# Kernel tuning notes

Hardware: AMD Instinct MI355X
Metric: run time of the kernel (lower is better)

The kernel has to match this reference:

```python
import jax, jax.numpy as jnp
import numpy as np

DIM = 2048
N_HEADS = 32
N_KV_HEADS = 8
HEAD_DIM = DIM // N_HEADS  # 64
N_REP = N_HEADS // N_KV_HEADS  # 4
B, S = 2, 2048
MASK_VAL = -32768.0


def setup_inputs() -> dict:
    key = jax.random.key(0)
    ks = jax.random.split(key, 7)
    x = jax.random.normal(ks[0], (B, S, DIM), dtype=jnp.float32)
    freqs_cos = jax.random.uniform(ks[1], (S, HEAD_DIM // 2), dtype=jnp.float32)
    freqs_sin = jax.random.uniform(ks[2], (S, HEAD_DIM // 2), dtype=jnp.float32)
    sc = 1.0 / np.sqrt(DIM)
    wq = jax.random.normal(ks[3], (N_HEADS * HEAD_DIM, DIM), dtype=jnp.float32) * sc
    wk = jax.random.normal(ks[4], (N_KV_HEADS * HEAD_DIM, DIM), dtype=jnp.float32) * sc
    wv = jax.random.normal(ks[5], (N_KV_HEADS * HEAD_DIM, DIM), dtype=jnp.float32) * sc
    wo = jax.random.normal(ks[6], (DIM, N_HEADS * HEAD_DIM), dtype=jnp.float32) * sc
    return {"x": x, "freqs_cos": freqs_cos, "freqs_sin": freqs_sin,
            "wq": wq, "wk": wk, "wv": wv, "wo": wo}


def _apply_rope(q, k, cos, sin):
    # q: [B,S,H,D], k: [B,S,Hkv,D]; interleaved real/imag pairs in last dim
    def rot(t):
        tr = t.reshape(t.shape[:-1] + (-1, 2))  # [..., D/2, 2]
        t_r, t_i = tr[..., 0], tr[..., 1]
        c = cos[None, :, None, :]  # broadcast over batch and heads
        s = sin[None, :, None, :]
        o_r = t_r * c - t_i * s
        o_i = t_r * s + t_i * c
        return jnp.stack([o_r, o_i], axis=-1).reshape(t.shape)
    return rot(q), rot(k)


def reference(x, freqs_cos, freqs_sin, wq, wk, wv, wo):
    bsz, seqlen, _ = x.shape
    xq = (x @ wq.T).reshape(bsz, seqlen, N_HEADS, HEAD_DIM)
    xk = (x @ wk.T).reshape(bsz, seqlen, N_KV_HEADS, HEAD_DIM)
    xv = (x @ wv.T).reshape(bsz, seqlen, N_KV_HEADS, HEAD_DIM)
    xq, xk = _apply_rope(xq, xk, freqs_cos, freqs_sin)
    # GQA: repeat each kv head n_rep times contiguously (matches per-head cat loop)
    xk = jnp.repeat(xk, N_REP, axis=2)  # [B,S,H,D]
    xv = jnp.repeat(xv, N_REP, axis=2)
    # [B,H,S,D]
    q = xq.transpose(0, 2, 1, 3)
    k = xk.transpose(0, 2, 1, 3)
    v = xv.transpose(0, 2, 1, 3)
    scores = jnp.einsum('bhqd,bhkd->bhqk', q, k) / jnp.sqrt(jnp.float32(HEAD_DIM))
    causal = jnp.triu(jnp.full((seqlen, seqlen), MASK_VAL, dtype=scores.dtype), k=1)
    scores = scores + causal[None, None, :, :]
    probs = jax.nn.softmax(scores.astype(jnp.float32), axis=-1).astype(q.dtype)
    out = jnp.einsum('bhqk,bhkd->bhqd', probs, v)
    out = out.transpose(0, 2, 1, 3).reshape(bsz, seqlen, -1)
    return out @ wo.T
```

## Files before the change

kernel.cpp:

```cpp
#include <hip/hip_runtime.h>
#include <hip/hip_bf16.h>
#include <type_traits>

typedef __bf16 bf16;
typedef __bf16 bf16x2 __attribute__((ext_vector_type(2)));
typedef __bf16 bf16x4 __attribute__((ext_vector_type(4)));
typedef __bf16 bf16x8 __attribute__((ext_vector_type(8)));
typedef float f32x4 __attribute__((ext_vector_type(4)));

#define AS1 __attribute__((address_space(1)))
#define AS3 __attribute__((address_space(3)))

#define KAPPA 0.180336880111f

__device__ __forceinline__ void load_lds16(const void* g, void* l) {
  __builtin_amdgcn_global_load_lds((AS1 void*)g, (AS3 void*)l, 16, 0, 0);
}
__device__ __forceinline__ float exp2_fast(float x) {
  return __builtin_amdgcn_exp2f(x);
}

__global__ void f2b_all(const float* __restrict__ x, const float* __restrict__ wq,
                        const float* __restrict__ wk, const float* __restrict__ wv,
                        const float* __restrict__ wo, bf16* __restrict__ xb,
                        bf16* __restrict__ wqkv, bf16* __restrict__ wob) {
  int bid = blockIdx.x;
  const float* src;
  bf16* dst;
  int off;
  if (bid < 8192) { src = x; dst = xb; off = bid; }
  else if (bid < 12288) { src = wq; dst = wqkv; off = bid - 8192; }
  else if (bid < 13312) { src = wk; dst = wqkv + 4194304; off = bid - 12288; }
  else if (bid < 14336) { src = wv; dst = wqkv + 5242880; off = bid - 13312; }
  else { src = wo; dst = wob; off = bid - 14336; }
  int i = (off * 256 + threadIdx.x) * 4;
  float4 v = *(const float4*)(src + i);
  bf16x4 o = {(bf16)v.x, (bf16)v.y, (bf16)v.z, (bf16)v.w};
  *(bf16x4*)(dst + i) = o;
}

__global__ __launch_bounds__(512, 2) void gemm_qkv(const bf16* __restrict__ A,
                                                   const bf16* __restrict__ Bw,
                                                   const float* __restrict__ fc,
                                                   const float* __restrict__ fs,
                                                   bf16* __restrict__ Qro,
                                                   bf16* __restrict__ Kro,
                                                   bf16* __restrict__ Vt) {
  const int K = 2048;
  __shared__ bf16 As[4][256][32];
  __shared__ bf16 Bs[4][256][32];
  const int t = threadIdx.x;
  const int wave = t >> 6, lane = t & 63, qd = lane >> 4, ln = lane & 15;
  const int wm = (wave >> 2) * 128;
  const int wn = (wave & 3) * 64;
  const int bn = blockIdx.x;
  const int bmrow = blockIdx.y * 256;

  const bf16* Ab = A + (size_t)bmrow * K;
  const bf16* Bb = Bw + (size_t)bn * 256 * K;

  auto stage = [&](const bf16* gb, char* lb, int tk, int sub) {
    int e = sub * 512 + t;
    int ro = e >> 2, gs = (e & 3) ^ (ro & 3);
    load_lds16(gb + (size_t)ro * K + tk * 32 + gs * 8,
               lb + (tk & 3) * 16384 + sub * 8192 + wave * 1024);
  };

#pragma unroll
  for (int tt = 0; tt < 3; tt++) {
    stage(Ab, (char*)As, tt, 0);
    stage(Ab, (char*)As, tt, 1);
    stage(Bb, (char*)Bs, tt, 0);
    stage(Bb, (char*)Bs, tt, 1);
  }
  asm volatile("s_waitcnt vmcnt(8)" ::: "memory");
  __builtin_amdgcn_s_barrier();

  f32x4 acc[8][4] = {};
  bf16x8 bfr[4];
  const int segoff = (qd ^ (ln & 3)) << 4;

  for (int tk = 0; tk < 64; tk++) {
    const char* Asl = (const char*)As + (tk & 3) * 16384;
    const char* Bsl = (const char*)Bs + (tk & 3) * 16384;

    bf16x8 af[4];
#pragma unroll
    for (int i = 0; i < 4; i++)
      af[i] = *(const bf16x8*)(Asl + (wm + i * 16 + ln) * 64 + segoff);
#pragma unroll
    for (int j = 0; j < 4; j++)
      bfr[j] = *(const bf16x8*)(Bsl + (wn + j * 16 + ln) * 64 + segoff);
    if (tk + 3 < 64) {
      stage(Ab, (char*)As, tk + 3, 0);
      stage(Ab, (char*)As, tk + 3, 1);
    }
    __builtin_amdgcn_s_barrier();
    asm volatile("s_waitcnt lgkmcnt(0)" ::: "memory");
    __builtin_amdgcn_sched_barrier(0);
    __builtin_amdgcn_s_setprio(1);
#pragma unroll
    for (int i = 0; i < 4; i++)
#pragma unroll
      for (int j = 0; j < 4; j++)
        acc[i][j] = __builtin_amdgcn_mfma_f32_16x16x32_bf16(af[i], bfr[j],
                                                            acc[i][j], 0, 0, 0);
    __builtin_amdgcn_s_setprio(0);
    __builtin_amdgcn_s_barrier();

#pragma unroll
    for (int i = 0; i < 4; i++)
      af[i] = *(const bf16x8*)(Asl + (wm + 64 + i * 16 + ln) * 64 + segoff);
    if (tk + 3 < 64) {
      stage(Bb, (char*)Bs, tk + 3, 0);
      stage(Bb, (char*)Bs, tk + 3, 1);
    }
    if (tk < 61) asm volatile("s_waitcnt vmcnt(8)" ::: "memory");
    else if (tk == 61) asm volatile("s_waitcnt vmcnt(4)" ::: "memory");
    else asm volatile("s_waitcnt vmcnt(0)" ::: "memory");
    __builtin_amdgcn_s_barrier();
    asm volatile("s_waitcnt lgkmcnt(0)" ::: "memory");
    __builtin_amdgcn_sched_barrier(0);
    __builtin_amdgcn_s_setprio(1);
#pragma unroll
    for (int i = 0; i < 4; i++)
#pragma unroll
      for (int j = 0; j < 4; j++)
        acc[4 + i][j] = __builtin_amdgcn_mfma_f32_16x16x32_bf16(
            af[i], bfr[j], acc[4 + i][j], 0, 0, 0);
    __builtin_amdgcn_s_setprio(0);
    __builtin_amdgcn_s_barrier();
  }

  const int b = bmrow >> 11;
  const int sb = (bmrow & 2047) + wm;
  const bool odd = ln & 1;

  if (bn < 10) {
    const bool isQ = bn < 8;
    const float kap = isQ ? KAPPA : 1.0f;
    const int h = (isQ ? bn : bn - 8) * 4 + (wave & 3);
    bf16* dst = isQ ? (Qro + (size_t)(b * 32 + h) * 2048 * 64)
                    : (Kro + (size_t)(b * 8 + h) * 2048 * 64);
#pragma unroll
    for (int i = 0; i < 8; i++) {
#pragma unroll
      for (int j = 0; j < 4; j++) {
        const int d = j * 16 + ln;
        const int i_f = d >> 1;
#pragma unroll
        for (int r = 0; r < 4; r++) {
          int s = sb + i * 16 + qd * 4 + r;
          float v = acc[i][j][r];
          float p = __shfl_xor(v, 1);
          float cv = fc[s * 32 + i_f] * kap;
          float sv = fs[s * 32 + i_f] * kap;
          float o = odd ? (p * sv + v * cv) : (v * cv - p * sv);
          dst[(size_t)s * 64 + d] = (bf16)o;
        }
      }
    }
  } else {
    const int kh = (bn - 10) * 4 + (wave & 3);
#pragma unroll
    for (int i = 0; i < 8; i++)
#pragma unroll
      for (int j = 0; j < 4; j++) {
        const int d = j * 16 + ln;
        int s = sb + i * 16 + qd * 4;
        bf16x4 ov = {(bf16)acc[i][j][0], (bf16)acc[i][j][1],
                     (bf16)acc[i][j][2], (bf16)acc[i][j][3]};
        *(bf16x4*)&Vt[((size_t)(b * 8 + kh) * 64 + d) * 2048 + s] = ov;
      }
  }
}

template <typename OutT>
__global__ __launch_bounds__(256, 4) void gemm_bt64(const bf16* __restrict__ A,
                                                    const bf16* __restrict__ Bw,
                                                    OutT* __restrict__ C,
                                                    int M, int N, int K) {
  __shared__ bf16 As[64][64];
  __shared__ bf16 Bs[128][64];
  const int t = threadIdx.x;
  const int wave = t >> 6, lane = t & 63, qd = lane >> 4, ln = lane & 15;
  const int wm = (wave >> 1) * 32;
  const int wn = (wave & 1) * 64;
  const size_t bm = (size_t)blockIdx.y * 64;
  const size_t bn = (size_t)blockIdx.x * 128;

  const bf16* Ab = A + bm * (size_t)K;
  const bf16* Bb = Bw + bn * (size_t)K;

  f32x4 acc[2][4] = {};

  for (int k0 = 0; k0 < K; k0 += 64) {
#pragma unroll
    for (int i = 0; i < 2; i++) {
      int e = i * 256 + t;
      int ro = e >> 3, gs = (e & 7) ^ (ro & 7);
      load_lds16(Ab + (size_t)ro * K + k0 + gs * 8,
                 (char*)As + i * 4096 + wave * 1024);
    }
#pragma unroll
    for (int i = 0; i < 4; i++) {
      int e = i * 256 + t;
      int ro = e >> 3, gs = (e & 7) ^ (ro & 7);
      load_lds16(Bb + (size_t)ro * K + k0 + gs * 8,
                 (char*)Bs + i * 4096 + wave * 1024);
    }
    __syncthreads();

#pragma unroll
    for (int kk = 0; kk < 2; kk++) {
      bf16x8 af[2], bfr[4];
#pragma unroll
      for (int i = 0; i < 2; i++) {
        int row = wm + i * 16 + ln;
        int ps = (kk * 4 + qd) ^ (row & 7);
        af[i] = *(const bf16x8*)((const char*)As + row * 128 + ps * 16);
      }
#pragma unroll
      for (int j = 0; j < 4; j++) {
        int row = wn + j * 16 + ln;
        int ps = (kk * 4 + qd) ^ (row & 7);
        bfr[j] = *(const bf16x8*)((const char*)Bs + row * 128 + ps * 16);
      }
#pragma unroll
      for (int i = 0; i < 2; i++)
#pragma unroll
        for (int j = 0; j < 4; j++)
          acc[i][j] = __builtin_amdgcn_mfma_f32_16x16x32_bf16(af[i], bfr[j],
                                                              acc[i][j], 0, 0, 0);
    }
    __syncthreads();
  }

#pragma unroll
  for (int i = 0; i < 2; i++)
#pragma unroll
    for (int j = 0; j < 4; j++)
#pragma unroll
      for (int r = 0; r < 4; r++) {
        size_t row = bm + wm + i * 16 + qd * 4 + r;
        size_t col = bn + wn + j * 16 + ln;
        C[row * N + col] = (OutT)acc[i][j][r];
      }
}

__global__ __launch_bounds__(256, 3) void attn_fwd(const bf16* __restrict__ Q,
                                                   const bf16* __restrict__ Kg,
                                                   const bf16* __restrict__ Vg,
                                                   bf16* __restrict__ O) {
  __shared__ bf16 Qs[128][64];
  __shared__ bf16 Ks[64][64];
  __shared__ bf16 Vs[64][64];
  __shared__ bf16 Ps[128][64];
  const int t = threadIdx.x;
  const int wave = t >> 6, lane = t & 63, qd = lane >> 4, ln = lane & 15;
  const int bid = blockIdx.x;
  const int qt = 15 - (bid >> 6);
  const int bh = bid & 63;
  const int b = bh >> 5, h = bh & 31, kh = h >> 2;
  const bf16* Qb = Q + ((size_t)(b * 32 + h) * 2048 + qt * 128) * 64;
  const bf16* Kb = Kg + (size_t)(b * 8 + kh) * 2048 * 64;
  const bf16* Vb = Vg + (size_t)(b * 8 + kh) * 64 * 2048;
  char* PsB = (char*)Ps;

#pragma unroll
  for (int i = 0; i < 4; i++) {
    int e = i * 256 + t;
    int row = e >> 3, sg = (e & 7) ^ (row & 7);
    load_lds16(Qb + (size_t)row * 64 + sg * 8, (char*)Qs + i * 4096 + wave * 1024);
  }

  f32x4 o_acc[4][2] = {};
  float l_st[2] = {0.f, 0.f};
  const int q0 = qt * 128 + wave * 32;
  const int nkb = 2 * qt + 2;

  for (int kb = 0; kb < nkb; kb++) {
    __syncthreads();
#pragma unroll
    for (int i = 0; i < 2; i++) {
      int e = i * 256 + t;
      int row = e >> 3, sg = (e & 7) ^ (row & 7);
      load_lds16(Kb + (size_t)(kb * 64 + row) * 64 + sg * 8,
                 (char*)Ks + i * 4096 + wave * 1024);
      load_lds16(Vb + (size_t)row * 2048 + kb * 64 + sg * 8,
                 (char*)Vs + i * 4096 + wave * 1024);
    }
    __syncthreads();

    f32x4 s_acc[4][2] = {};
#pragma unroll
    for (int kk = 0; kk < 2; kk++) {
      bf16x8 ak[4], bq[2];
#pragma unroll
      for (int j = 0; j < 4; j++) {
        int row = j * 16 + ln;
        int ph = (kk * 4 + qd) ^ (ln & 7);
        ak[j] = *(const bf16x8*)((const char*)Ks + row * 128 + ph * 16);
      }
#pragma unroll
      for (int mi = 0; mi < 2; mi++) {
        int row = wave * 32 + mi * 16 + ln;
        int ph = (kk * 4 + qd) ^ (ln & 7);
        bq[mi] = *(const bf16x8*)((const char*)Qs + row * 128 + ph * 16);
      }
#pragma unroll
      for (int j = 0; j < 4; j++)
#pragma unroll
        for (int mi = 0; mi < 2; mi++)
          s_acc[j][mi] = __builtin_amdgcn_mfma_f32_16x16x32_bf16(
              ak[j], bq[mi], s_acc[j][mi], 0, 0, 0);
    }

    auto smax = [&](auto maskc) {
      constexpr bool MASK = decltype(maskc)::value;
#pragma unroll
      for (int mi = 0; mi < 2; mi++) {
        const int qv = q0 + mi * 16 + ln;
        const int prow = wave * 32 + mi * 16 + ln;
        float rs = 0.f;
#pragma unroll
        for (int j = 0; j < 4; j++) {
          bf16x4 pk;
#pragma unroll
          for (int r = 0; r < 4; r++) {
            float s = s_acc[j][mi][r];
            if (MASK) {
              int k_glob = kb * 64 + j * 16 + qd * 4 + r;
              if (k_glob > qv) s = -1e5f;
            }
            float pv = exp2_fast(s - 16.f);
            rs += pv;
            pk[r] = (bf16)pv;
          }
          int ps = (j * 2 + (qd >> 1)) ^ (ln & 7);
          *(bf16x4*)(PsB + prow * 128 + ps * 16 + (qd & 1) * 8) = pk;
        }
        l_st[mi] += rs;
      }
    };
    if (kb * 64 + 63 > q0) smax(std::true_type{});
    else smax(std::false_type{});

#pragma unroll
    for (int kk = 0; kk < 2; kk++) {
      bf16x8 av[4], bp[2];
#pragma unroll
      for (int dj = 0; dj < 4; dj++) {
        int row = dj * 16 + ln;
        int ph = (kk * 4 + qd) ^ (ln & 7);
        av[dj] = *(const bf16x8*)((const char*)Vs + row * 128 + ph * 16);
      }
#pragma unroll
      for (int mi = 0; mi < 2; mi++) {
        int prow = wave * 32 + mi * 16 + ln;
        int ph = (kk * 4 + qd) ^ (ln & 7);
        bp[mi] = *(const bf16x8*)(PsB + prow * 128 + ph * 16);
      }
#pragma unroll
      for (int dj = 0; dj < 4; dj++)
#pragma unroll
        for (int mi = 0; mi < 2; mi++)
          o_acc[dj][mi] = __builtin_amdgcn_mfma_f32_16x16x32_bf16(
              av[dj], bp[mi], o_acc[dj][mi], 0, 0, 0);
    }
  }

#pragma unroll
  for (int mi = 0; mi < 2; mi++) {
    float lt = l_st[mi];
    lt += __shfl_xor(lt, 16);
    lt += __shfl_xor(lt, 32);
    float inv = 1.f / lt;
    int q_idx = qt * 128 + wave * 32 + mi * 16 + ln;
#pragma unroll
    for (int dj = 0; dj < 4; dj++) {
      bf16x4 ov;
#pragma unroll
      for (int r = 0; r < 4; r++) ov[r] = (bf16)(o_acc[dj][mi][r] * inv);
      *(bf16x4*)&O[((size_t)(b * 2048 + q_idx) * 32 + h) * 64 + dj * 16 + qd * 4] = ov;
    }
  }
}

extern "C" void kernel_launch(void* const* d_in, const int* in_sizes, int n_in,
                              void* d_out, int out_size, void* d_ws,
                              size_t ws_size, hipStream_t stream) {
  const float* x = (const float*)d_in[0];
  const float* fc = (const float*)d_in[1];
  const float* fs = (const float*)d_in[2];
  const float* wq = (const float*)d_in[3];
  const float* wk = (const float*)d_in[4];
  const float* wv = (const float*)d_in[5];
  const float* wo = (const float*)d_in[6];
  float* out = (float*)d_out;

  char* ws = (char*)d_ws;
  const size_t MB = (size_t)1 << 20;
  bf16* xb   = (bf16*)(ws + 0 * MB);
  bf16* wqkv = (bf16*)(ws + 16 * MB);
  bf16* wob  = (bf16*)(ws + 28 * MB);
  bf16* Qro  = (bf16*)(ws + 36 * MB);
  bf16* Kro  = (bf16*)(ws + 52 * MB);
  bf16* Vt   = (bf16*)(ws + 56 * MB);
  bf16* Oa   = (bf16*)(ws + 60 * MB);

  dim3 blk(256);
  f2b_all<<<18432, blk, 0, stream>>>(x, wq, wk, wv, wo, xb, wqkv, wob);
  gemm_qkv<<<dim3(12, 16), dim3(512), 0, stream>>>(xb, wqkv, fc, fs, Qro, Kro, Vt);
  attn_fwd<<<1024, blk, 0, stream>>>(Qro, Kro, Vt, Oa);
  gemm_bt64<float><<<dim3(16, 64), blk, 0, stream>>>(Oa, wob, out, 4096, 2048, 2048);
}
```

Baseline: 293.3 us.

## Shrink QKV GEMM N-tile to 192 to fill more CUs and change LDS swizzle

Result: faster. 273.8 us (-6.7%).

```diff
diff --git a/kernel.cpp b/kernel.cpp
--- a/kernel.cpp
+++ b/kernel.cpp
@@ -48,52 +48,61 @@
                                                    bf16* __restrict__ Vt) {
   const int K = 2048;
   __shared__ bf16 As[4][256][32];
-  __shared__ bf16 Bs[4][256][32];
+  __shared__ bf16 Bs[4][192][32];
   const int t = threadIdx.x;
   const int wave = t >> 6, lane = t & 63, qd = lane >> 4, ln = lane & 15;
   const int wm = (wave >> 2) * 128;
-  const int wn = (wave & 3) * 64;
+  const int wn = (wave & 3) * 48;
   const int bn = blockIdx.x;
   const int bmrow = blockIdx.y * 256;
 
   const bf16* Ab = A + (size_t)bmrow * K;
-  const bf16* Bb = Bw + (size_t)bn * 256 * K;
-
-  auto stage = [&](const bf16* gb, char* lb, int tk, int sub) {
+  const bf16* Bb = Bw + (size_t)bn * 192 * K;
+
+  auto stageA = [&](int tk, int sub) {
     int e = sub * 512 + t;
-    int ro = e >> 2, gs = (e & 3) ^ (ro & 3);
-    load_lds16(gb + (size_t)ro * K + tk * 32 + gs * 8,
-               lb + (tk & 3) * 16384 + sub * 8192 + wave * 1024);
+    int ro = e >> 2, gs = (e & 3) ^ ((ro >> 1) & 3);
+    load_lds16(Ab + (size_t)ro * K + tk * 32 + gs * 8,
+               (char*)As + (tk & 3) * 16384 + sub * 8192 + wave * 1024);
   };
+  auto stageB = [&](int tk, int sub) {
+    if (sub == 0 || t < 256) {
+      int e = sub * 512 + t;
+      int ro = e >> 2, gs = (e & 3) ^ ((ro >> 1) & 3);
+      load_lds16(Bb + (size_t)ro * K + tk * 32 + gs * 8,
+                 (char*)Bs + (tk & 3) * 12288 + sub * 8192 + wave * 1024);
+    }
+  };
 
 #pragma unroll
   for (int tt = 0; tt < 3; tt++) {
-    stage(Ab, (char*)As, tt, 0);
-    stage(Ab, (char*)As, tt, 1);
-    stage(Bb, (char*)Bs, tt, 0);
-    stage(Bb, (char*)Bs, tt, 1);
-  }
-  asm volatile("s_waitcnt vmcnt(8)" ::: "memory");
+    stageA(tt, 0);
+    stageA(tt, 1);
+    stageB(tt, 0);
+    stageB(tt, 1);
+  }
+  if (wave < 4) asm volatile("s_waitcnt vmcnt(8)" ::: "memory");
+  else         asm volatile("s_waitcnt vmcnt(6)" ::: "memory");
   __builtin_amdgcn_s_barrier();
 
-  f32x4 acc[8][4] = {};
-  bf16x8 bfr[4];
-  const int segoff = (qd ^ (ln & 3)) << 4;
+  f32x4 acc[8][3] = {};
+  bf16x8 bfr[3];
+  const int segoff = (qd ^ ((ln >> 1) & 3)) << 4;
 
   for (int tk = 0; tk < 64; tk++) {
     const char* Asl = (const char*)As + (tk & 3) * 16384;
-    const char* Bsl = (const char*)Bs + (tk & 3) * 16384;
+    const char* Bsl = (const char*)Bs + (tk & 3) * 12288;
 
     bf16x8 af[4];
 #pragma unroll
     for (int i = 0; i < 4; i++)
       af[i] = *(const bf16x8*)(Asl + (wm + i * 16 + ln) * 64 + segoff);
 #pragma unroll
-    for (int j = 0; j < 4; j++)
+    for (int j = 0; j < 3; j++)
       bfr[j] = *(const bf16x8*)(Bsl + (wn + j * 16 + ln) * 64 + segoff);
     if (tk + 3 < 64) {
-      stage(Ab, (char*)As, tk + 3, 0);
-      stage(Ab, (char*)As, tk + 3, 1);
+      stageA(tk + 3, 0);
+      stageA(tk + 3, 1);
     }
     __builtin_amdgcn_s_barrier();
     asm volatile("s_waitcnt lgkmcnt(0)" ::: "memory");
@@ -102,7 +111,7 @@
 #pragma unroll
     for (int i = 0; i < 4; i++)
 #pragma unroll
-      for (int j = 0; j < 4; j++)
+      for (int j = 0; j < 3; j++)
         acc[i][j] = __builtin_amdgcn_mfma_f32_16x16x32_bf16(af[i], bfr[j],
                                                             acc[i][j], 0, 0, 0);
     __builtin_amdgcn_s_setprio(0);
@@ -112,12 +121,18 @@
     for (int i = 0; i < 4; i++)
       af[i] = *(const bf16x8*)(Asl + (wm + 64 + i * 16 + ln) * 64 + segoff);
     if (tk + 3 < 64) {
-      stage(Bb, (char*)Bs, tk + 3, 0);
-      stage(Bb, (char*)Bs, tk + 3, 1);
-    }
-    if (tk < 61) asm volatile("s_waitcnt vmcnt(8)" ::: "memory");
-    else if (tk == 61) asm volatile("s_waitcnt vmcnt(4)" ::: "memory");
-    else asm volatile("s_waitcnt vmcnt(0)" ::: "memory");
+      stageB(tk + 3, 0);
+      stageB(tk + 3, 1);
+    }
+    if (tk < 61) {
+      if (wave < 4) asm volatile("s_waitcnt vmcnt(8)" ::: "memory");
+      else         asm volatile("s_waitcnt vmcnt(6)" ::: "memory");
+    } else if (tk == 61) {
+      if (wave < 4) asm volatile("s_waitcnt vmcnt(4)" ::: "memory");
+      else         asm volatile("s_waitcnt vmcnt(3)" ::: "memory");
+    } else {
+      asm volatile("s_waitcnt vmcnt(0)" ::: "memory");
+    }
     __builtin_amdgcn_s_barrier();
     asm volatile("s_waitcnt lgkmcnt(0)" ::: "memory");
     __builtin_amdgcn_sched_barrier(0);
@@ -125,7 +140,7 @@
 #pragma unroll
     for (int i = 0; i < 4; i++)
 #pragma unroll
-      for (int j = 0; j < 4; j++)
+      for (int j = 0; j < 3; j++)
         acc[4 + i][j] = __builtin_amdgcn_mfma_f32_16x16x32_bf16(
             af[i], bfr[j], acc[4 + i][j], 0, 0, 0);
     __builtin_amdgcn_s_setprio(0);
@@ -136,18 +151,19 @@
   const int sb = (bmrow & 2047) + wm;
   const bool odd = ln & 1;
 
-  if (bn < 10) {
-    const bool isQ = bn < 8;
-    const float kap = isQ ? KAPPA : 1.0f;
-    const int h = (isQ ? bn : bn - 8) * 4 + (wave & 3);
-    bf16* dst = isQ ? (Qro + (size_t)(b * 32 + h) * 2048 * 64)
-                    : (Kro + (size_t)(b * 8 + h) * 2048 * 64);
-#pragma unroll
-    for (int i = 0; i < 8; i++) {
-#pragma unroll
-      for (int j = 0; j < 4; j++) {
-        const int d = j * 16 + ln;
-        const int i_f = d >> 1;
+#pragma unroll
+  for (int j = 0; j < 3; j++) {
+    const int cbase = bn * 192 + wn + j * 16;
+    const int hg = cbase >> 6;
+    const int d = (cbase & 63) + ln;
+    if (hg < 40) {
+      const bool isQ = hg < 32;
+      const float kap = isQ ? KAPPA : 1.0f;
+      bf16* dst = isQ ? (Qro + (size_t)(b * 32 + hg) * 2048 * 64)
+                      : (Kro + (size_t)(b * 8 + (hg - 32)) * 2048 * 64);
+      const int i_f = d >> 1;
+#pragma unroll
+      for (int i = 0; i < 8; i++) {
 #pragma unroll
         for (int r = 0; r < 4; r++) {
           int s = sb + i * 16 + qd * 4 + r;
@@ -159,19 +175,16 @@
           dst[(size_t)s * 64 + d] = (bf16)o;
         }
       }
-    }
-  } else {
-    const int kh = (bn - 10) * 4 + (wave & 3);
-#pragma unroll
-    for (int i = 0; i < 8; i++)
-#pragma unroll
-      for (int j = 0; j < 4; j++) {
-        const int d = j * 16 + ln;
+    } else {
+      const int kh = hg - 40;
+#pragma unroll
+      for (int i = 0; i < 8; i++) {
         int s = sb + i * 16 + qd * 4;
         bf16x4 ov = {(bf16)acc[i][j][0], (bf16)acc[i][j][1],
                      (bf16)acc[i][j][2], (bf16)acc[i][j][3]};
         *(bf16x4*)&Vt[((size_t)(b * 8 + kh) * 64 + d) * 2048 + s] = ov;
       }
+    }
   }
 }
 
@@ -411,7 +424,7 @@
 
   dim3 blk(256);
   f2b_all<<<18432, blk, 0, stream>>>(x, wq, wk, wv, wo, xb, wqkv, wob);
-  gemm_qkv<<<dim3(12, 16), dim3(512), 0, stream>>>(xb, wqkv, fc, fs, Qro, Kro, Vt);
+  gemm_qkv<<<dim3(16, 16), dim3(512), 0, stream>>>(xb, wqkv, fc, fs, Qro, Kro, Vt);
   attn_fwd<<<1024, blk, 0, stream>>>(Qro, Kro, Vt, Oa);
   gemm_bt64<float><<<dim3(16, 64), blk, 0, stream>>>(Oa, wob, out, 4096, 2048, 2048);
 }
```

## Merge two-phase GEMM k-loop into single phase and change LDS swizzle

Applied to the files above, without the earlier changes.

New measurement: 295.8 us. Within noise of the previous version (+0.9%).

```diff
diff --git a/kernel.cpp b/kernel.cpp
--- a/kernel.cpp
+++ b/kernel.cpp
@@ -59,76 +59,59 @@
   const bf16* Ab = A + (size_t)bmrow * K;
   const bf16* Bb = Bw + (size_t)bn * 256 * K;
 
-  auto stage = [&](const bf16* gb, char* lb, int tk, int sub) {
+  auto stage1 = [&](const bf16* gb, char* lb, int tk, int sub) {
     int e = sub * 512 + t;
-    int ro = e >> 2, gs = (e & 3) ^ (ro & 3);
+    int ro = e >> 2, gs = (e & 3) ^ ((ro >> 1) & 3);
     load_lds16(gb + (size_t)ro * K + tk * 32 + gs * 8,
                lb + (tk & 3) * 16384 + sub * 8192 + wave * 1024);
   };
 
 #pragma unroll
   for (int tt = 0; tt < 3; tt++) {
-    stage(Ab, (char*)As, tt, 0);
-    stage(Ab, (char*)As, tt, 1);
-    stage(Bb, (char*)Bs, tt, 0);
-    stage(Bb, (char*)Bs, tt, 1);
+    stage1(Ab, (char*)As, tt, 0);
+    stage1(Ab, (char*)As, tt, 1);
+    stage1(Bb, (char*)Bs, tt, 0);
+    stage1(Bb, (char*)Bs, tt, 1);
   }
   asm volatile("s_waitcnt vmcnt(8)" ::: "memory");
   __builtin_amdgcn_s_barrier();
 
   f32x4 acc[8][4] = {};
-  bf16x8 bfr[4];
-  const int segoff = (qd ^ (ln & 3)) << 4;
+  const int segoff = (qd ^ ((ln >> 1) & 3)) << 4;
 
   for (int tk = 0; tk < 64; tk++) {
     const char* Asl = (const char*)As + (tk & 3) * 16384;
     const char* Bsl = (const char*)Bs + (tk & 3) * 16384;
 
-    bf16x8 af[4];
-#pragma unroll
-    for (int i = 0; i < 4; i++)
+    if (tk + 3 < 64) {
+      stage1(Ab, (char*)As, tk + 3, 0);
+      stage1(Ab, (char*)As, tk + 3, 1);
+      stage1(Bb, (char*)Bs, tk + 3, 0);
+      stage1(Bb, (char*)Bs, tk + 3, 1);
+    }
+
+    bf16x8 af[8], bfr[4];
+#pragma unroll
+    for (int i = 0; i < 8; i++)
       af[i] = *(const bf16x8*)(Asl + (wm + i * 16 + ln) * 64 + segoff);
 #pragma unroll
     for (int j = 0; j < 4; j++)
       bfr[j] = *(const bf16x8*)(Bsl + (wn + j * 16 + ln) * 64 + segoff);
-    if (tk + 3 < 64) {
-      stage(Ab, (char*)As, tk + 3, 0);
-      stage(Ab, (char*)As, tk + 3, 1);
-    }
-    __builtin_amdgcn_s_barrier();
+
     asm volatile("s_waitcnt lgkmcnt(0)" ::: "memory");
     __builtin_amdgcn_sched_barrier(0);
     __builtin_amdgcn_s_setprio(1);
 #pragma unroll
-    for (int i = 0; i < 4; i++)
+    for (int i = 0; i < 8; i++)
 #pragma unroll
       for (int j = 0; j < 4; j++)
         acc[i][j] = __builtin_amdgcn_mfma_f32_16x16x32_bf16(af[i], bfr[j],
                                                             acc[i][j], 0, 0, 0);
     __builtin_amdgcn_s_setprio(0);
-    __builtin_amdgcn_s_barrier();
-
-#pragma unroll
-    for (int i = 0; i < 4; i++)
-      af[i] = *(const bf16x8*)(Asl + (wm + 64 + i * 16 + ln) * 64 + segoff);
-    if (tk + 3 < 64) {
-      stage(Bb, (char*)Bs, tk + 3, 0);
-      stage(Bb, (char*)Bs, tk + 3, 1);
-    }
+
     if (tk < 61) asm volatile("s_waitcnt vmcnt(8)" ::: "memory");
     else if (tk == 61) asm volatile("s_waitcnt vmcnt(4)" ::: "memory");
-    else asm volatile("s_waitcnt vmcnt(0)" ::: "memory");
-    __builtin_amdgcn_s_barrier();
-    asm volatile("s_waitcnt lgkmcnt(0)" ::: "memory");
-    __builtin_amdgcn_sched_barrier(0);
-    __builtin_amdgcn_s_setprio(1);
-#pragma unroll
-    for (int i = 0; i < 4; i++)
-#pragma unroll
-      for (int j = 0; j < 4; j++)
-        acc[4 + i][j] = __builtin_amdgcn_mfma_f32_16x16x32_bf16(
-            af[i], bfr[j], acc[4 + i][j], 0, 0, 0);
-    __builtin_amdgcn_s_setprio(0);
+    else if (tk == 62) asm volatile("s_waitcnt vmcnt(0)" ::: "memory");
     __builtin_amdgcn_s_barrier();
   }
 
```

## Double-buffer K/V tiles in attention, keep Q in registers, retune GEMM LDS swizzle

Applied to the files above, without the earlier changes.

Result: faster. 275.1 us (-6.2%).

```diff
diff --git a/kernel.cpp b/kernel.cpp
--- a/kernel.cpp
+++ b/kernel.cpp
@@ -59,26 +59,26 @@
   const bf16* Ab = A + (size_t)bmrow * K;
   const bf16* Bb = Bw + (size_t)bn * 256 * K;
 
-  auto stage = [&](const bf16* gb, char* lb, int tk, int sub) {
+  auto stage1 = [&](const bf16* gb, char* lb, int tk, int sub) {
     int e = sub * 512 + t;
-    int ro = e >> 2, gs = (e & 3) ^ (ro & 3);
+    int ro = e >> 2, gs = (e & 3) ^ ((ro >> 1) & 3);
     load_lds16(gb + (size_t)ro * K + tk * 32 + gs * 8,
                lb + (tk & 3) * 16384 + sub * 8192 + wave * 1024);
   };
 
 #pragma unroll
   for (int tt = 0; tt < 3; tt++) {
-    stage(Ab, (char*)As, tt, 0);
-    stage(Ab, (char*)As, tt, 1);
-    stage(Bb, (char*)Bs, tt, 0);
-    stage(Bb, (char*)Bs, tt, 1);
+    stage1(Ab, (char*)As, tt, 0);
+    stage1(Ab, (char*)As, tt, 1);
+    stage1(Bb, (char*)Bs, tt, 0);
+    stage1(Bb, (char*)Bs, tt, 1);
   }
   asm volatile("s_waitcnt vmcnt(8)" ::: "memory");
   __builtin_amdgcn_s_barrier();
 
   f32x4 acc[8][4] = {};
   bf16x8 bfr[4];
-  const int segoff = (qd ^ (ln & 3)) << 4;
+  const int segoff = (qd ^ ((ln >> 1) & 3)) << 4;
 
   for (int tk = 0; tk < 64; tk++) {
     const char* Asl = (const char*)As + (tk & 3) * 16384;
@@ -92,8 +92,8 @@
     for (int j = 0; j < 4; j++)
       bfr[j] = *(const bf16x8*)(Bsl + (wn + j * 16 + ln) * 64 + segoff);
     if (tk + 3 < 64) {
-      stage(Ab, (char*)As, tk + 3, 0);
-      stage(Ab, (char*)As, tk + 3, 1);
+      stage1(Ab, (char*)As, tk + 3, 0);
+      stage1(Ab, (char*)As, tk + 3, 1);
     }
     __builtin_amdgcn_s_barrier();
     asm volatile("s_waitcnt lgkmcnt(0)" ::: "memory");
@@ -112,8 +112,8 @@
     for (int i = 0; i < 4; i++)
       af[i] = *(const bf16x8*)(Asl + (wm + 64 + i * 16 + ln) * 64 + segoff);
     if (tk + 3 < 64) {
-      stage(Bb, (char*)Bs, tk + 3, 0);
-      stage(Bb, (char*)Bs, tk + 3, 1);
+      stage1(Bb, (char*)Bs, tk + 3, 0);
+      stage1(Bb, (char*)Bs, tk + 3, 1);
     }
     if (tk < 61) asm volatile("s_waitcnt vmcnt(8)" ::: "memory");
     else if (tk == 61) asm volatile("s_waitcnt vmcnt(4)" ::: "memory");
@@ -252,9 +252,8 @@
                                                    const bf16* __restrict__ Kg,
                                                    const bf16* __restrict__ Vg,
                                                    bf16* __restrict__ O) {
-  __shared__ bf16 Qs[128][64];
-  __shared__ bf16 Ks[64][64];
-  __shared__ bf16 Vs[64][64];
+  __shared__ bf16 Ks[2][64][64];
+  __shared__ bf16 Vs[2][64][64];
   __shared__ bf16 Ps[128][64];
   const int t = threadIdx.x;
   const int wave = t >> 6, lane = t & 63, qd = lane >> 4, ln = lane & 15;
@@ -267,53 +266,56 @@
   const bf16* Vb = Vg + (size_t)(b * 8 + kh) * 64 * 2048;
   char* PsB = (char*)Ps;
 
-#pragma unroll
-  for (int i = 0; i < 4; i++) {
-    int e = i * 256 + t;
-    int row = e >> 3, sg = (e & 7) ^ (row & 7);
-    load_lds16(Qb + (size_t)row * 64 + sg * 8, (char*)Qs + i * 4096 + wave * 1024);
-  }
+  bf16x8 qf[2][2];
+#pragma unroll
+  for (int kk = 0; kk < 2; kk++)
+#pragma unroll
+    for (int mi = 0; mi < 2; mi++)
+      qf[kk][mi] = *(const bf16x8*)(Qb + (wave * 32 + mi * 16 + ln) * 64 +
+                                    (kk * 4 + qd) * 8);
+
+  auto stageKV = [&](int kb, int buf) {
+#pragma unroll
+    for (int i = 0; i < 2; i++) {
+      int e = i * 256 + t;
+      int row = e >> 3, sg = (e & 7) ^ (row & 7);
+      load_lds16(Kb + (size_t)(kb * 64 + row) * 64 + sg * 8,
+                 (char*)Ks + buf * 8192 + i * 4096 + wave * 1024);
+      load_lds16(Vb + (size_t)row * 2048 + kb * 64 + sg * 8,
+                 (char*)Vs + buf * 8192 + i * 4096 + wave * 1024);
+    }
+  };
 
   f32x4 o_acc[4][2] = {};
   float l_st[2] = {0.f, 0.f};
   const int q0 = qt * 128 + wave * 32;
   const int nkb = 2 * qt + 2;
 
+  stageKV(0, 0);
+  __syncthreads();
+
   for (int kb = 0; kb < nkb; kb++) {
-    __syncthreads();
-#pragma unroll
-    for (int i = 0; i < 2; i++) {
-      int e = i * 256 + t;
-      int row = e >> 3, sg = (e & 7) ^ (row & 7);
-      load_lds16(Kb + (size_t)(kb * 64 + row) * 64 + sg * 8,
-                 (char*)Ks + i * 4096 + wave * 1024);
-      load_lds16(Vb + (size_t)row * 2048 + kb * 64 + sg * 8,
-                 (char*)Vs + i * 4096 + wave * 1024);
-    }
-    __syncthreads();
+    const int cur = kb & 1;
+    if (kb + 1 < nkb) stageKV(kb + 1, cur ^ 1);
+    const char* Ksl = (const char*)Ks + cur * 8192;
+    const char* Vsl = (const char*)Vs + cur * 8192;
 
     f32x4 s_acc[4][2] = {};
 #pragma unroll
     for (int kk = 0; kk < 2; kk++) {
-      bf16x8 ak[4], bq[2];
+      bf16x8 ak[4];
 #pragma unroll
       for (int j = 0; j < 4; j++) {
         int row = j * 16 + ln;
         int ph = (kk * 4 + qd) ^ (ln & 7);
-        ak[j] = *(const bf16x8*)((const char*)Ks + row * 128 + ph * 16);
-      }
-#pragma unroll
-      for (int mi = 0; mi < 2; mi++) {
-        int row = wave * 32 + mi * 16 + ln;
-        int ph = (kk * 4 + qd) ^ (ln & 7);
-        bq[mi] = *(const bf16x8*)((const char*)Qs + row * 128 + ph * 16);
+        ak[j] = *(const bf16x8*)(Ksl + row * 128 + ph * 16);
       }
 #pragma unroll
       for (int j = 0; j < 4; j++)
 #pragma unroll
         for (int mi = 0; mi < 2; mi++)
           s_acc[j][mi] = __builtin_amdgcn_mfma_f32_16x16x32_bf16(
-              ak[j], bq[mi], s_acc[j][mi], 0, 0, 0);
+              ak[j], qf[kk][mi], s_acc[j][mi], 0, 0, 0);
     }
 
     auto smax = [&](auto maskc) {
@@ -353,7 +355,7 @@
       for (int dj = 0; dj < 4; dj++) {
         int row = dj * 16 + ln;
         int ph = (kk * 4 + qd) ^ (ln & 7);
-        av[dj] = *(const bf16x8*)((const char*)Vs + row * 128 + ph * 16);
+        av[dj] = *(const bf16x8*)(Vsl + row * 128 + ph * 16);
       }
 #pragma unroll
       for (int mi = 0; mi < 2; mi++) {
@@ -368,6 +370,8 @@
           o_acc[dj][mi] = __builtin_amdgcn_mfma_f32_16x16x32_bf16(
               av[dj], bp[mi], o_acc[dj][mi], 0, 0, 0);
     }
+
+    __syncthreads();
   }
 
 #pragma unroll
```
